# Performance work log

Measured on AMD Instinct MI355X. Metric: run time of the kernel, lower is better.

The kernel has to match this reference:

```python
import jax, jax.numpy as jnp
import numpy as np
import math

B, C_IN, C_OUT, H, W = 16, 128, 128, 56, 56
K, S, P, D = 3, 1, 1, 1
PROD_KS = K * K


def _unfold(x, k, s, p, d):
    # torch.nn.functional.unfold equivalent -> (B, k*k, C, Ho*Wo)
    b, c, h, w = x.shape
    ho = (h + 2 * p - d * (k - 1) - 1) // s + 1
    wo = (w + 2 * p - d * (k - 1) - 1) // s + 1
    xp = jnp.pad(x, ((0, 0), (0, 0), (p, p), (p, p)))
    patches = [
        xp[:, :, i * d: i * d + (ho - 1) * s + 1: s, j * d: j * d + (wo - 1) * s + 1: s]
        for i in range(k) for j in range(k)
    ]
    u = jnp.stack(patches, axis=1)  # (B, K2, C, Ho, Wo)
    return u.reshape(b, k * k, c, ho * wo), ho, wo


def setup_inputs() -> dict:
    key = jax.random.key(0)
    k1, k2, k3, k4 = jax.random.split(key, 4)
    stdv = 1.0 / math.sqrt(C_IN * PROD_KS)
    x = jax.random.normal(k1, (B, C_IN, H, W), dtype=jnp.float32)
    weight = jax.random.uniform(k2, (1, PROD_KS, C_OUT, C_IN), dtype=jnp.float32,
                                minval=-stdv, maxval=stdv)
    b_k = jax.random.uniform(k3, (1, PROD_KS, 1, C_OUT, 1), dtype=jnp.float32,
                             minval=-stdv, maxval=stdv)
    bias = jax.random.uniform(k4, (C_OUT,), dtype=jnp.float32, minval=-stdv, maxval=stdv)
    return {"x": x, "weight": weight, "b_k": b_k, "bias": bias}


def reference(x, weight, b_k, bias):
    batch = x.shape[0]
    u, ho, wo = _unfold(x, K, S, P, D)          # (B, K2, C_in, L)
    inpt = u.transpose(0, 1, 3, 2)               # (B, K2, L, C_in)
    # GEMM: (B,K2,L,Cin) x (K2,Cout,Cin) -> (B,K2,L,Cout)
    out = jnp.einsum('bklc,koc->bklo', inpt, weight[0])
    bk = b_k[0, :, 0, :, 0]                      # (K2, Cout)
    # fused cos/sin contraction over kernel positions -> (B, L, Cout) each
    a = jnp.einsum('bklo,ko->blo', out, jnp.cos(bk))
    bb = jnp.einsum('bklo,ko->blo', out, jnp.sin(bk))
    eps = 1e-05
    a_gt = a > 0
    b_gt = bb > 0
    ab_eq = a_gt == b_gt
    theta = jnp.where(ab_eq, jnp.arctan(bb / (a + eps)), -jnp.arctan(a / (bb + eps)))
    pi = math.pi
    peak = jnp.where(ab_eq & a_gt, pi / 2.0,
           jnp.where(ab_eq & ~a_gt, -pi / 2.0,
           jnp.where(~ab_eq & ~b_gt, -pi, 0.0)))
    theta = peak - theta
    o = jnp.sin(theta) * a + jnp.cos(theta) * bb  # (B, L, Cout)
    o = o.transpose(0, 2, 1) + bias[None, :, None]  # (B, Cout, L)
    conv_out = o.reshape(batch, C_OUT, ho, wo)
    theta_out = (theta / pi).transpose(0, 2, 1).reshape(batch, C_OUT, ho, wo)
    return jnp.concatenate([conv_out, theta_out], axis=1)
```

## Files before the change

### kernel.cpp

```cpp
#include <hip/hip_runtime.h>
#include <hip/hip_bf16.h>
#include <math.h>

#define NB   16
#define CIN  128
#define COUT 128
#define HH   56
#define WW   56
#define LL   3136

typedef __attribute__((ext_vector_type(8))) short short8;
typedef __attribute__((ext_vector_type(16))) float f32x16;
typedef __attribute__((ext_vector_type(4))) float f32x4;
typedef __attribute__((ext_vector_type(4))) unsigned int uint4v;

#define PXT    256
#define NPXT   13
#define XC     58
#define XRR    8
#define QN     (XRR*XC)
#define XPLANE 7424
#define XUSH   14848
#define XUNITS 1856
#define XHALF  928
#define CPW    16
#define WS_TAP 1024
#define WS_N   9216
#define WUSH   18432
#define WBYTES 36864
#define SMUSH  (XUSH + WUSH)

#define XT_ROWS 62
#define XT_PLANE_USH (XT_ROWS*XC*16)
#define XT_CG_STRIDE 3682304

#define CSD_OFF 256
#define WSP_OFF 32768
#define XT_OFF  1212416
#define XT_SIZE 29458432
#define WL_OFF  (XT_OFF + XT_SIZE)

__global__ void prep_csd_kernel(const float* __restrict__ bk, double* __restrict__ csd) {
    int i = blockIdx.x * 256 + threadIdx.x;
    if (i < 2*9*COUT) {
        int s = i / (9*COUT);
        int rem = i - s*(9*COUT);
        double v = (double)bk[rem];
        csd[i] = (s == 0) ? cos(v) : sin(v);
    }
}

__global__ void prep_w_kernel(const float* __restrict__ w, const double* __restrict__ csd,
                              unsigned short* __restrict__ wsp) {
    int i = blockIdx.x * 256 + threadIdx.x;
    if (i >= 9*COUT*CIN) return;
    int k = i / (COUT*CIN);
    int rem = i - k*(COUT*CIN);
    int oc = rem >> 7, c = rem & 127;
    double ck = csd[k*COUT + oc];
    double sk = csd[9*COUT + k*COUT + oc];
    float wv = w[i];
    float fa = (float)(ck * (double)wv);
    float fb = (float)(sk * (double)wv);
    __hip_bfloat16 ah = __float2bfloat16(fa);
    __hip_bfloat16 al = __float2bfloat16(fa - __bfloat162float(ah));
    __hip_bfloat16 bh = __float2bfloat16(fb);
    __hip_bfloat16 bl = __float2bfloat16(fb - __bfloat162float(bh));
    int ocb = oc >> 5;
    int rowa = oc & 31, rowb = 32 + rowa;
    int cg = c >> 4, cp = c & 15;
    int sl = (((cp >> 3) ^ ((rowa >> 2) & 1)) << 3) | (cp & 7);
    size_t img = ((size_t)ocb*8 + cg) * WUSH;
    wsp[img + (size_t)k*WS_TAP + rowa*CPW + sl]        = *(unsigned short*)&ah;
    wsp[img + (size_t)k*WS_TAP + rowb*CPW + sl]        = *(unsigned short*)&bh;
    wsp[img + WS_N + (size_t)k*WS_TAP + rowa*CPW + sl] = *(unsigned short*)&al;
    wsp[img + WS_N + (size_t)k*WS_TAP + rowb*CPW + sl] = *(unsigned short*)&bl;
}

__global__ void prep_x_kernel(const float* __restrict__ x, unsigned short* __restrict__ xt) {
    int i = blockIdx.x * 256 + threadIdx.x;
    int c58 = i % XC;
    int t = i / XC;
    int row = t % XT_ROWS;
    t /= XT_ROWS;
    int bat = t & 15;
    int cg  = t >> 4;
    int gr = row - 1, gc = c58 - 1;
    bool valid = ((unsigned)gr < HH) && ((unsigned)gc < WW);
    unsigned short hi[16], lo[16];
    #pragma unroll
    for (int j = 0; j < 16; j++) {
        float v = 0.f;
        if (valid) v = x[(size_t)(bat*CIN + cg*16 + j)*LL + gr*WW + gc];
        __hip_bfloat16 h = __float2bfloat16(v);
        __hip_bfloat16 l = __float2bfloat16(v - __bfloat162float(h));
        hi[j] = *(unsigned short*)&h;
        lo[j] = *(unsigned short*)&l;
    }
    size_t base = ((((size_t)cg*16 + bat)*2 + 0)*XT_ROWS + row)*XC + c58;
    unsigned short* dh = xt + base*16;
    unsigned short* dl = dh + XT_PLANE_USH;
    *(uint4v*)dh       = *(const uint4v*)&hi[0];
    *(uint4v*)(dh + 8) = *(const uint4v*)&hi[8];
    *(uint4v*)dl       = *(const uint4v*)&lo[0];
    *(uint4v*)(dl + 8) = *(const uint4v*)&lo[8];
}

__global__ __launch_bounds__(256, 2)
void mfma_kernel(const unsigned short* __restrict__ xt, const unsigned short* __restrict__ wsp,
                 const float* __restrict__ bias, float* __restrict__ out,
                 unsigned* __restrict__ cnt, unsigned* __restrict__ wl, unsigned cap)
{
    __shared__ __align__(16) unsigned short SM[SMUSH];
    __shared__ float sm_bias[32];

    const int tid = threadIdx.x;
    int bid = blockIdx.x;
    int wk = (bid & 7) * (NB*NPXT*4/8) + (bid >> 3);
    const int ocb = wk & 3; wk >>= 2;
    const int pxt = wk % NPXT;
    const int bat = wk / NPXT;
    const int l0  = pxt * PXT;
    const int o0  = ocb * 32;
    const int yf  = l0 / WW;

    const int lane = tid & 63;
    const int n    = lane & 31;
    const int kh   = lane >> 5;
    const int wave = tid >> 6;

    if (tid < 32) sm_bias[tid] = bias[o0 + tid];

    unsigned xoff[8];
    #pragma unroll
    for (int k = 0; k < 8; k++) {
        int u = tid + 256*k;
        int uc = u < XUNITS ? u : XUNITS-1;
        int pl = uc >= XHALF ? 1 : 0;
        int rem = uc - pl*XHALF;
        int q  = rem >> 1;
        int hl = rem & 1;
        int hg = hl ^ ((q >> 2) & 1);
        int r  = q / XC;
        int c  = q - r*XC;
        xoff[k] = (unsigned)((((bat*2 + pl)*XT_ROWS + (yf + r))*XC + c)*32 + hg*16);
    }

    int q0g[2];
    #pragma unroll
    for (int g = 0; g < 2; g++) {
        int p  = l0 + wave*64 + g*32 + n;
        int pc = p < LL ? p : LL-1;
        int py = pc / WW, pxx = pc - py*WW;
        q0g[g] = (py - yf)*XC + pxx;
    }
    const int sw  = ((((n>>2)&1) ^ kh) << 3);
    const int iAa = n*CPW + sw;
    const int iAb = (32+n)*CPW + sw;

    f32x16 acc_a[2], acc_b[2];
    #pragma unroll
    for (int g = 0; g < 2; g++) {
        #pragma unroll
        for (int r = 0; r < 16; r++) { acc_a[g][r] = 0.f; acc_b[g][r] = 0.f; }
    }

    const char* xtB  = (const char*)xt;
    const char* wspB = (const char*)wsp + (size_t)ocb * (8*WBYTES);

    uint4v xpf[8], wpf[9];

    auto load_stage = [&](int chn) {
        const char* xp = xtB + (size_t)chn * XT_CG_STRIDE;
        #pragma unroll
        for (int k = 0; k < 8; k++) xpf[k] = *(const uint4v*)(xp + xoff[k]);
        const char* wp = wspB + (size_t)chn * WBYTES + tid*16;
        #pragma unroll
        for (int k = 0; k < 9; k++) wpf[k] = *(const uint4v*)(wp + k*4096);
    };
    auto write_stage = [&]() {
        #pragma unroll
        for (int k = 0; k < 7; k++) *(uint4v*)&SM[(tid + 256*k)*8] = xpf[k];
        if (tid < (XUNITS - 1792)) *(uint4v*)&SM[(tid + 1792)*8] = xpf[7];
        #pragma unroll
        for (int k = 0; k < 9; k++) *(uint4v*)&SM[XUSH + (tid + 256*k)*8] = wpf[k];
    };

    load_stage(0);
    write_stage();
    __syncthreads();
    load_stage(1);

    #pragma unroll 1
    for (int ch = 0; ch < 8; ch++) {
        #pragma unroll
        for (int tap = 0; tap < 9; tap++) {
            const int ky = tap / 3, kx = tap - 3*ky;
            const int wb = XUSH + tap*WS_TAP;
            short8 Aha = *(const short8*)&SM[wb + iAa];
            short8 Ahb = *(const short8*)&SM[wb + iAb];
            short8 Ala = *(const short8*)&SM[wb + WS_N + iAa];
            short8 Alb = *(const short8*)&SM[wb + WS_N + iAb];
            #pragma unroll
            for (int g = 0; g < 2; g++) {
                int q  = q0g[g] + ky*XC + kx;
                int si = q*16 + ((kh ^ ((q>>2)&1)) << 3);
                short8 Bh = *(const short8*)&SM[si];
                short8 Bl = *(const short8*)&SM[XPLANE + si];
                acc_a[g] = __builtin_amdgcn_mfma_f32_32x32x16_bf16(Ala, Bh, acc_a[g], 0,0,0);
                acc_a[g] = __builtin_amdgcn_mfma_f32_32x32x16_bf16(Aha, Bl, acc_a[g], 0,0,0);
                acc_a[g] = __builtin_amdgcn_mfma_f32_32x32x16_bf16(Aha, Bh, acc_a[g], 0,0,0);
                acc_b[g] = __builtin_amdgcn_mfma_f32_32x32x16_bf16(Alb, Bh, acc_b[g], 0,0,0);
                acc_b[g] = __builtin_amdgcn_mfma_f32_32x32x16_bf16(Ahb, Bl, acc_b[g], 0,0,0);
                acc_b[g] = __builtin_amdgcn_mfma_f32_32x32x16_bf16(Ahb, Bh, acc_b[g], 0,0,0);
            }
        }
        if (ch < 7) {
            __syncthreads();
            write_stage();
            __syncthreads();
            if (ch < 6) load_stage(ch + 2);
        }
    }

    __syncthreads();
    float* conv_s  = (float*)SM;
    float* theta_s = conv_s + 32*PXT;
    const float eps = 1e-05f;
    const float PIf = 3.14159265358979323846f;

    #pragma unroll
    for (int g = 0; g < 2; g++) {
        const int pcol = wave*64 + g*32 + n;
        const int p = l0 + pcol;
        #pragma unroll
        for (int r = 0; r < 16; r++) {
            int row = (r & 3) + 8*(r >> 2) + 4*kh;
            float av = acc_a[g][r];
            float bv = acc_b[g][r];
            bool flag = (p < LL) &&
                        (fabsf(av) < 1.5e-4f || (bv < 1.05e-5f && bv > -2.05e-5f));
            unsigned long long m = __ballot(flag);
            if (m) {
                int leader = (int)__ffsll((long long)m) - 1;
                unsigned base = 0;
                if (lane == leader) base = atomicAdd(cnt, (unsigned)__popcll(m));
                base = __shfl(base, leader);
                if (flag) {
                    unsigned slot = base + (unsigned)__popcll(m & ((1ULL << lane) - 1ULL));
                    if (slot < cap)
                        wl[slot] = ((unsigned)(bat*LL + p) << 7) | (unsigned)(o0 + row);
                }
            }
            bool ag = av > 0.f, bg = bv > 0.f;
            bool eq = (ag == bg);
            float ratio = eq ? (bv / (av + eps)) : (av / (bv + eps));
            float at = atanf(ratio);
            if (!eq) at = -at;
            float peak = eq ? (ag ? PIf*0.5f : -PIf*0.5f) : (bg ? 0.0f : -PIf);
            float th = peak - at;
            conv_s[row*PXT + pcol]  = sinf(th)*av + cosf(th)*bv + sm_bias[row];
            theta_s[row*PXT + pcol] = th * (1.0f/PIf);
        }
    }
    __syncthreads();
    size_t obase = (size_t)bat * (2*COUT) * LL;
    #pragma unroll
    for (int i = 0; i < 8; i++) {
        int s = tid + 256*i;
        int row = s >> 6, seg = s & 63;
        int px0 = l0 + seg*4;
        if (px0 < LL)
            *(f32x4*)&out[obase + (size_t)(o0+row)*LL + px0] = *(const f32x4*)&conv_s[(row<<8) + (seg<<2)];
    }
    #pragma unroll
    for (int i = 0; i < 8; i++) {
        int s = tid + 256*i;
        int row = s >> 6, seg = s & 63;
        int px0 = l0 + seg*4;
        if (px0 < LL)
            *(f32x4*)&out[obase + (size_t)(COUT+o0+row)*LL + px0] = *(const f32x4*)&theta_s[(row<<8) + (seg<<2)];
    }
}

__global__ __launch_bounds__(256)
void fixup_kernel(const float* __restrict__ x, const float* __restrict__ w,
                  const double* __restrict__ csd, const float* __restrict__ bias,
                  const unsigned* __restrict__ cnt, const unsigned* __restrict__ wl,
                  unsigned cap, float* __restrict__ out) {
    const int lane   = threadIdx.x & 63;
    const int waveid = (blockIdx.x * 256 + threadIdx.x) >> 6;
    const int nwaves = gridDim.x * 4;
    unsigned nf = *cnt; if (nf > cap) nf = cap;
    const double PI = 3.14159265358979323846;

    for (unsigned u = waveid; u < nf; u += nwaves) {
        unsigned idx = wl[u];
        int oc = idx & 127;
        unsigned rest = idx >> 7;
        int bb_ = rest / LL;
        int l   = rest - bb_*LL;
        int yy  = l / WW;
        int xx  = l - yy*WW;
        const float* xb = x + (size_t)bb_ * CIN * LL;

        double pa = 0.0, pb = 0.0;
        #pragma unroll
        for (int k = 0; k < 9; k++) {
            int dy = k/3, dx = k - dy*3;
            int py = yy + dy - 1, px = xx + dx - 1;
            double pk = 0.0;
            if ((unsigned)py < HH && (unsigned)px < WW) {
                int base = py*WW + px;
                const float* wr = w + k*(COUT*CIN) + oc*CIN;
                int c = lane;
                pk  = (double)xb[(size_t)c*LL + base] * (double)wr[c];
                c = lane + 64;
                pk += (double)xb[(size_t)c*LL + base] * (double)wr[c];
            }
            pa += csd[k*COUT + oc] * pk;
            pb += csd[9*COUT + k*COUT + oc] * pk;
        }
        #pragma unroll
        for (int off = 32; off > 0; off >>= 1) {
            pa += __shfl_xor(pa, off, 64);
            pb += __shfl_xor(pb, off, 64);
        }
        if (lane == 0) {
            bool ag = pa > 0.0, bg = pb > 0.0;
            bool eq = (ag == bg);
            double th;
            if (eq) th = (ag ? PI*0.5 : -PI*0.5) - atan(pb / (pa + 1e-5));
            else    th = (bg ? 0.0 : -PI) + atan(pa / (pb + 1e-5));
            double o = sin(th)*pa + cos(th)*pb + (double)bias[oc];
            out[((size_t)bb_*(2*COUT) + oc) * LL + l]        = (float)o;
            out[((size_t)bb_*(2*COUT) + COUT + oc) * LL + l] = (float)(th / PI);
        }
    }
}

extern "C" void kernel_launch(void* const* d_in, const int* in_sizes, int n_in,
                              void* d_out, int out_size, void* d_ws, size_t ws_size,
                              hipStream_t stream) {
    const float* x    = (const float*)d_in[0];
    const float* w    = (const float*)d_in[1];
    const float* bk   = (const float*)d_in[2];
    const float* bias = (const float*)d_in[3];
    float* out = (float*)d_out;

    char* ws = (char*)d_ws;
    unsigned*       cnt = (unsigned*)ws;
    double*         csd = (double*)(ws + CSD_OFF);
    unsigned short* wsp = (unsigned short*)(ws + WSP_OFF);
    unsigned short* xt  = (unsigned short*)(ws + XT_OFF);
    unsigned*       wl  = (unsigned*)(ws + WL_OFF);
    unsigned cap = (ws_size > (size_t)WL_OFF + 4096) ? (unsigned)((ws_size - WL_OFF) / 4) : 0u;

    hipMemsetAsync(cnt, 0, 4, stream);
    hipLaunchKernelGGL(prep_csd_kernel, dim3(9),    dim3(256), 0, stream, bk, csd);
    hipLaunchKernelGGL(prep_w_kernel,   dim3(576),  dim3(256), 0, stream, w, csd, wsp);
    hipLaunchKernelGGL(prep_x_kernel,   dim3(1798), dim3(256), 0, stream, x, xt);
    hipLaunchKernelGGL(mfma_kernel,     dim3(NB*NPXT*4), dim3(256), 0, stream,
                       xt, wsp, bias, out, cnt, wl, cap);
    hipLaunchKernelGGL(fixup_kernel,    dim3(512),  dim3(256), 0, stream,
                       x, w, csd, bias, cnt, wl, cap, out);
}
```

Measured before the change: 338.0 us.

## Stream weights from global to registers, DMA x into LDS, fuse prep kernels

Merges the cos/sin prep into the weight prep kernel, which drops one launch. The x prep kernel now reads float4 vectors and writes only the zero border separately. The main kernel keeps only the x tile in LDS, loaded directly with global_load_lds. Weights are read from global memory (L2) into double-buffered registers per tap, which frees LDS so launch bounds can rise to 3 blocks per SM. The kernel also adds s_setprio around the MFMAs and writes outputs straight from registers instead of staging them in LDS, trading coalesced float4 stores for scalar strided stores and relying on L2 for repeated weight reads.

```diff
diff --git a/kernel.cpp b/kernel.cpp
--- a/kernel.cpp
+++ b/kernel.cpp
@@ -17,8 +17,6 @@
 #define PXT    256
 #define NPXT   13
 #define XC     58
-#define XRR    8
-#define QN     (XRR*XC)
 #define XPLANE 7424
 #define XUSH   14848
 #define XUNITS 1856
@@ -26,9 +24,7 @@
 #define CPW    16
 #define WS_TAP 1024
 #define WS_N   9216
-#define WUSH   18432
 #define WBYTES 36864
-#define SMUSH  (XUSH + WUSH)
 
 #define XT_ROWS 62
 #define XT_PLANE_USH (XT_ROWS*XC*16)
@@ -40,25 +36,19 @@
 #define XT_SIZE 29458432
 #define WL_OFF  (XT_OFF + XT_SIZE)
 
-__global__ void prep_csd_kernel(const float* __restrict__ bk, double* __restrict__ csd) {
-    int i = blockIdx.x * 256 + threadIdx.x;
-    if (i < 2*9*COUT) {
-        int s = i / (9*COUT);
-        int rem = i - s*(9*COUT);
-        double v = (double)bk[rem];
-        csd[i] = (s == 0) ? cos(v) : sin(v);
-    }
-}
-
-__global__ void prep_w_kernel(const float* __restrict__ w, const double* __restrict__ csd,
-                              unsigned short* __restrict__ wsp) {
+__global__ void prep_w_kernel(const float* __restrict__ w, const float* __restrict__ bk,
+                              double* __restrict__ csd, unsigned short* __restrict__ wsp) {
     int i = blockIdx.x * 256 + threadIdx.x;
     if (i >= 9*COUT*CIN) return;
     int k = i / (COUT*CIN);
     int rem = i - k*(COUT*CIN);
     int oc = rem >> 7, c = rem & 127;
-    double ck = csd[k*COUT + oc];
-    double sk = csd[9*COUT + k*COUT + oc];
+    double bkv = (double)bk[k*COUT + oc];
+    double ck = cos(bkv), sk = sin(bkv);
+    if (c == 0) {
+        csd[k*COUT + oc]          = ck;
+        csd[9*COUT + k*COUT + oc] = sk;
+    }
     float wv = w[i];
     float fa = (float)(ck * (double)wv);
     float fb = (float)(sk * (double)wv);
@@ -70,7 +60,7 @@
     int rowa = oc & 31, rowb = 32 + rowa;
     int cg = c >> 4, cp = c & 15;
     int sl = (((cp >> 3) ^ ((rowa >> 2) & 1)) << 3) | (cp & 7);
-    size_t img = ((size_t)ocb*8 + cg) * WUSH;
+    size_t img = ((size_t)ocb*8 + cg) * (WBYTES/2);
     wsp[img + (size_t)k*WS_TAP + rowa*CPW + sl]        = *(unsigned short*)&ah;
     wsp[img + (size_t)k*WS_TAP + rowb*CPW + sl]        = *(unsigned short*)&bh;
     wsp[img + WS_N + (size_t)k*WS_TAP + rowa*CPW + sl] = *(unsigned short*)&al;
@@ -79,39 +69,59 @@
 
 __global__ void prep_x_kernel(const float* __restrict__ x, unsigned short* __restrict__ xt) {
     int i = blockIdx.x * 256 + threadIdx.x;
-    int c58 = i % XC;
-    int t = i / XC;
-    int row = t % XT_ROWS;
-    t /= XT_ROWS;
-    int bat = t & 15;
-    int cg  = t >> 4;
-    int gr = row - 1, gc = c58 - 1;
-    bool valid = ((unsigned)gr < HH) && ((unsigned)gc < WW);
-    unsigned short hi[16], lo[16];
-    #pragma unroll
-    for (int j = 0; j < 16; j++) {
-        float v = 0.f;
-        if (valid) v = x[(size_t)(bat*CIN + cg*16 + j)*LL + gr*WW + gc];
-        __hip_bfloat16 h = __float2bfloat16(v);
-        __hip_bfloat16 l = __float2bfloat16(v - __bfloat162float(h));
-        hi[j] = *(unsigned short*)&h;
-        lo[j] = *(unsigned short*)&l;
-    }
-    size_t base = ((((size_t)cg*16 + bat)*2 + 0)*XT_ROWS + row)*XC + c58;
-    unsigned short* dh = xt + base*16;
-    unsigned short* dl = dh + XT_PLANE_USH;
-    *(uint4v*)dh       = *(const uint4v*)&hi[0];
-    *(uint4v*)(dh + 8) = *(const uint4v*)&hi[8];
-    *(uint4v*)dl       = *(const uint4v*)&lo[0];
-    *(uint4v*)(dl + 8) = *(const uint4v*)&lo[8];
-}
-
-__global__ __launch_bounds__(256, 2)
+    if (i < 100352) {
+        int c4 = i % 14; int t = i / 14;
+        int row1 = t % 56; t /= 56;
+        int bat = t & 15, cg = t >> 4;
+        const float* xp = x + ((size_t)(bat*CIN + cg*16))*LL + row1*WW + c4*4;
+        unsigned short hi[4][16], lo[4][16];
+        #pragma unroll
+        for (int j = 0; j < 16; j++) {
+            f32x4 v = *(const f32x4*)(xp + (size_t)j*LL);
+            #pragma unroll
+            for (int cc = 0; cc < 4; cc++) {
+                float f = v[cc];
+                __hip_bfloat16 h = __float2bfloat16(f);
+                __hip_bfloat16 l = __float2bfloat16(f - __bfloat162float(h));
+                hi[cc][j] = *(unsigned short*)&h;
+                lo[cc][j] = *(unsigned short*)&l;
+            }
+        }
+        size_t base = ((((size_t)cg*16 + bat)*2 + 0)*XT_ROWS + (row1+1))*XC + (c4*4 + 1);
+        #pragma unroll
+        for (int cc = 0; cc < 4; cc++) {
+            unsigned short* dh = xt + (base + cc)*16;
+            unsigned short* dl = dh + XT_PLANE_USH;
+            *(uint4v*)dh       = *(const uint4v*)&hi[cc][0];
+            *(uint4v*)(dh + 8) = *(const uint4v*)&hi[cc][8];
+            *(uint4v*)dl       = *(const uint4v*)&lo[cc][0];
+            *(uint4v*)(dl + 8) = *(const uint4v*)&lo[cc][8];
+        }
+    } else {
+        int i2 = i - 100352;
+        int unit = i2 % 460; int t = i2 / 460;
+        int pl = t & 1; t >>= 1;
+        int bat = t & 15, cg = t >> 4;
+        int row, c58;
+        if (unit < 348) {
+            int zr = unit / 58; c58 = unit - zr*58;
+            row = (zr == 0) ? 0 : (56 + zr);
+        } else {
+            int u2 = unit - 348; row = 1 + (u2 >> 1); c58 = (u2 & 1) ? 57 : 0;
+        }
+        size_t base = ((((size_t)cg*16 + bat)*2 + pl)*XT_ROWS + row)*XC + c58;
+        uint4v zz = {0u,0u,0u,0u};
+        *(uint4v*)(xt + base*16)     = zz;
+        *(uint4v*)(xt + base*16 + 8) = zz;
+    }
+}
+
+__global__ __launch_bounds__(256, 3)
 void mfma_kernel(const unsigned short* __restrict__ xt, const unsigned short* __restrict__ wsp,
                  const float* __restrict__ bias, float* __restrict__ out,
                  unsigned* __restrict__ cnt, unsigned* __restrict__ wl, unsigned cap)
 {
-    __shared__ __align__(16) unsigned short SM[SMUSH];
+    __shared__ __align__(16) unsigned short SM[XUSH];
     __shared__ float sm_bias[32];
 
     const int tid = threadIdx.x;
@@ -166,41 +176,49 @@
     }
 
     const char* xtB  = (const char*)xt;
-    const char* wspB = (const char*)wsp + (size_t)ocb * (8*WBYTES);
-
-    uint4v xpf[8], wpf[9];
-
-    auto load_stage = [&](int chn) {
+    const char* wspB = (const char*)wsp + (size_t)ocb * (8*(size_t)WBYTES);
+
+    auto stage = [&](int chn) {
         const char* xp = xtB + (size_t)chn * XT_CG_STRIDE;
         #pragma unroll
-        for (int k = 0; k < 8; k++) xpf[k] = *(const uint4v*)(xp + xoff[k]);
-        const char* wp = wspB + (size_t)chn * WBYTES + tid*16;
-        #pragma unroll
-        for (int k = 0; k < 9; k++) wpf[k] = *(const uint4v*)(wp + k*4096);
+        for (int k = 0; k < 7; k++) {
+            __builtin_amdgcn_global_load_lds(
+                (const __attribute__((address_space(1))) unsigned int*)(xp + xoff[k]),
+                (__attribute__((address_space(3))) unsigned int*)&SM[(wave*64 + 256*k)*8],
+                16, 0, 0);
+        }
+        if (wave == 0)
+            __builtin_amdgcn_global_load_lds(
+                (const __attribute__((address_space(1))) unsigned int*)(xp + xoff[7]),
+                (__attribute__((address_space(3))) unsigned int*)&SM[1792*8],
+                16, 0, 0);
     };
-    auto write_stage = [&]() {
-        #pragma unroll
-        for (int k = 0; k < 7; k++) *(uint4v*)&SM[(tid + 256*k)*8] = xpf[k];
-        if (tid < (XUNITS - 1792)) *(uint4v*)&SM[(tid + 1792)*8] = xpf[7];
-        #pragma unroll
-        for (int k = 0; k < 9; k++) *(uint4v*)&SM[XUSH + (tid + 256*k)*8] = wpf[k];
+
+    short8 wbuf[2][4];
+    auto ldw = [&](int chn, int tap, short8* dst) {
+        const char* tp = wspB + (size_t)chn*WBYTES + tap*(WS_TAP*2);
+        dst[0] = *(const short8*)(tp + iAa*2);
+        dst[1] = *(const short8*)(tp + iAb*2);
+        dst[2] = *(const short8*)(tp + 2*WS_N + iAa*2);
+        dst[3] = *(const short8*)(tp + 2*WS_N + iAb*2);
     };
 
-    load_stage(0);
-    write_stage();
+    stage(0);
+    ldw(0, 0, wbuf[0]);
+    ldw(0, 1, wbuf[1]);
     __syncthreads();
-    load_stage(1);
 
     #pragma unroll 1
     for (int ch = 0; ch < 8; ch++) {
         #pragma unroll
         for (int tap = 0; tap < 9; tap++) {
             const int ky = tap / 3, kx = tap - 3*ky;
-            const int wb = XUSH + tap*WS_TAP;
-            short8 Aha = *(const short8*)&SM[wb + iAa];
-            short8 Ahb = *(const short8*)&SM[wb + iAb];
-            short8 Ala = *(const short8*)&SM[wb + WS_N + iAa];
-            short8 Alb = *(const short8*)&SM[wb + WS_N + iAb];
+            short8 Aha = wbuf[tap&1][0];
+            short8 Ahb = wbuf[tap&1][1];
+            short8 Ala = wbuf[tap&1][2];
+            short8 Alb = wbuf[tap&1][3];
+            if (tap < 7) ldw(ch, tap+2, wbuf[tap&1]);
+            __builtin_amdgcn_s_setprio(1);
             #pragma unroll
             for (int g = 0; g < 2; g++) {
                 int q  = q0g[g] + ky*XC + kx;
@@ -214,20 +232,20 @@
                 acc_b[g] = __builtin_amdgcn_mfma_f32_32x32x16_bf16(Ahb, Bl, acc_b[g], 0,0,0);
                 acc_b[g] = __builtin_amdgcn_mfma_f32_32x32x16_bf16(Ahb, Bh, acc_b[g], 0,0,0);
             }
+            __builtin_amdgcn_s_setprio(0);
         }
         if (ch < 7) {
+            ldw(ch+1, 0, wbuf[0]);
+            ldw(ch+1, 1, wbuf[1]);
             __syncthreads();
-            write_stage();
+            stage(ch+1);
             __syncthreads();
-            if (ch < 6) load_stage(ch + 2);
-        }
-    }
-
-    __syncthreads();
-    float* conv_s  = (float*)SM;
-    float* theta_s = conv_s + 32*PXT;
+        }
+    }
+
     const float eps = 1e-05f;
     const float PIf = 3.14159265358979323846f;
+    size_t obase = (size_t)bat * (2*COUT) * LL;
 
     #pragma unroll
     for (int g = 0; g < 2; g++) {
@@ -259,27 +277,11 @@
             if (!eq) at = -at;
             float peak = eq ? (ag ? PIf*0.5f : -PIf*0.5f) : (bg ? 0.0f : -PIf);
             float th = peak - at;
-            conv_s[row*PXT + pcol]  = sinf(th)*av + cosf(th)*bv + sm_bias[row];
-            theta_s[row*PXT + pcol] = th * (1.0f/PIf);
-        }
-    }
-    __syncthreads();
-    size_t obase = (size_t)bat * (2*COUT) * LL;
-    #pragma unroll
-    for (int i = 0; i < 8; i++) {
-        int s = tid + 256*i;
-        int row = s >> 6, seg = s & 63;
-        int px0 = l0 + seg*4;
-        if (px0 < LL)
-            *(f32x4*)&out[obase + (size_t)(o0+row)*LL + px0] = *(const f32x4*)&conv_s[(row<<8) + (seg<<2)];
-    }
-    #pragma unroll
-    for (int i = 0; i < 8; i++) {
-        int s = tid + 256*i;
-        int row = s >> 6, seg = s & 63;
-        int px0 = l0 + seg*4;
-        if (px0 < LL)
-            *(f32x4*)&out[obase + (size_t)(COUT+o0+row)*LL + px0] = *(const f32x4*)&theta_s[(row<<8) + (seg<<2)];
+            if (p < LL) {
+                out[obase + (size_t)(o0+row)*LL + p]      = sinf(th)*av + cosf(th)*bv + sm_bias[row];
+                out[obase + (size_t)(COUT+o0+row)*LL + p] = th * (1.0f/PIf);
+            }
+        }
     }
 }
 
@@ -357,9 +359,8 @@
     unsigned cap = (ws_size > (size_t)WL_OFF + 4096) ? (unsigned)((ws_size - WL_OFF) / 4) : 0u;
 
     hipMemsetAsync(cnt, 0, 4, stream);
-    hipLaunchKernelGGL(prep_csd_kernel, dim3(9),    dim3(256), 0, stream, bk, csd);
-    hipLaunchKernelGGL(prep_w_kernel,   dim3(576),  dim3(256), 0, stream, w, csd, wsp);
-    hipLaunchKernelGGL(prep_x_kernel,   dim3(1798), dim3(256), 0, stream, x, xt);
+    hipLaunchKernelGGL(prep_w_kernel,   dim3(576),  dim3(256), 0, stream, w, bk, csd, wsp);
+    hipLaunchKernelGGL(prep_x_kernel,   dim3(852),  dim3(256), 0, stream, x, xt);
     hipLaunchKernelGGL(mfma_kernel,     dim3(NB*NPXT*4), dim3(256), 0, stream,
                        xt, wsp, bias, out, cnt, wl, cap);
     hipLaunchKernelGGL(fixup_kernel,    dim3(512),  dim3(256), 0, stream,
```

Result: no change. 335.2 us (-0.8%).
